# Kernel optimization log

Hardware: AMD Instinct MI355X
Metric: run time of the kernel (lower is better)

Reference implementation:

```python
import jax, jax.numpy as jnp
import numpy as np

STRIDE = 16
NUM_A = 9
POS_TH, NEG_TH = 0.7, 0.3
FG, BG, IGN = 1.0, 0.0, 2.0
CAP = 128  # BATCH_SIZE * 0.5 for both fg and bg


def _generate_base_anchors(base_size=16, ratios=(0.5, 1.0, 2.0), scales=(8, 16, 32)):
    w = h = float(base_size)
    xc = yc = 0.5 * (base_size - 1)
    size = w * h
    out = []
    for r in ratios:
        ws = np.round(np.sqrt(size / r))
        hs = np.round(ws * r)
        for s in scales:
            W, H = ws * s, hs * s
            out.append([xc - 0.5 * (W - 1), yc - 0.5 * (H - 1),
                        xc + 0.5 * (W - 1), yc + 0.5 * (H - 1)])
    return np.asarray(out, dtype=np.float32)  # [9,4]


def _all_anchors(H, W):
    base = _generate_base_anchors()
    sx = np.arange(W, dtype=np.float32) * STRIDE
    sy = np.arange(H, dtype=np.float32) * STRIDE
    xs, ys = np.meshgrid(sx, sy)  # row-major over (h, w)
    shifts = np.stack([xs.ravel(), ys.ravel(), xs.ravel(), ys.ravel()], 1)
    return jnp.asarray((shifts[:, None, :] + base[None, :, :]).reshape(-1, 4))  # [H*W*9,4], order (h,w,a)


def _forward(scores, gt, im_w, im_h):
    H, W = scores.shape[2], scores.shape[3]
    anchors = _all_anchors(H, W)  # [N,4]
    valid = (anchors[:, 0] >= 0.) & (anchors[:, 1] >= 0.) & \
            (anchors[:, 2] < im_w) & (anchors[:, 3] < im_h)
    # pairwise IoU with +1 box convention
    aw = anchors[:, 2] - anchors[:, 0] + 1.
    ah = anchors[:, 3] - anchors[:, 1] + 1.
    a_area = jnp.where((aw > 0) & (ah > 0), aw * ah, 0.)
    gw = gt[:, 2] - gt[:, 0] + 1.
    gh = gt[:, 3] - gt[:, 1] + 1.
    g_area = jnp.where((gw > 0) & (gh > 0), gw * gh, 0.)
    ix1 = jnp.maximum(anchors[:, None, 0], gt[None, :, 0])
    iy1 = jnp.maximum(anchors[:, None, 1], gt[None, :, 1])
    ix2 = jnp.minimum(anchors[:, None, 2], gt[None, :, 2])
    iy2 = jnp.minimum(anchors[:, None, 3], gt[None, :, 3])
    iw = ix2 - ix1 + 1.
    ih = iy2 - iy1 + 1.
    inter = jnp.where((iw > 0) & (ih > 0), iw * ih, 0.)
    ovl = inter / (a_area[:, None] + g_area[None, :] - inter)  # [N,G]
    ovl_m = jnp.where(valid[:, None], ovl, -1.)  # exclude invalid anchors
    a_argmax = jnp.argmax(ovl, axis=1)           # best gt per anchor
    a_max = jnp.max(ovl, axis=1)
    g_max = jnp.max(ovl_m, axis=0)               # best (valid) anchor overlap per gt
    gt_fg = jnp.any(ovl_m == g_max[None, :], axis=1) & valid
    labels = jnp.where(valid & (a_max < NEG_TH), BG, IGN)
    labels = jnp.where(gt_fg, FG, labels)
    labels = jnp.where(valid & (a_max >= POS_TH), FG, labels)
    # random subsample fg/bg down to CAP each (matches npr.choice semantics in distribution)
    kf, kb = jax.random.split(jax.random.key(42))
    def subsample(lbl, mask, k):
        s = jnp.where(mask, jax.random.uniform(k, lbl.shape), jnp.inf)
        ranks = jnp.argsort(jnp.argsort(s))
        keep = ranks < jnp.minimum(jnp.sum(mask), CAP)
        return jnp.where(mask & ~keep, IGN, lbl)
    labels = subsample(labels, labels == FG, kf)
    labels = subsample(labels, labels == BG, kb)
    num_ni = jnp.sum(labels != IGN).astype(jnp.float32)
    gts = gt[a_argmax]
    ax = (anchors[:, 2] + anchors[:, 0]) * 0.5
    ay = (anchors[:, 3] + anchors[:, 1]) * 0.5
    gwm = gts[:, 2] - gts[:, 0] + 1.
    ghm = gts[:, 3] - gts[:, 1] + 1.
    gx = (gts[:, 2] + gts[:, 0]) * 0.5
    gy = (gts[:, 3] + gts[:, 1]) * 0.5
    adj = jnp.stack([(gx - ax) / aw, (gy - ay) / ah,
                     jnp.log(gwm / aw), jnp.log(ghm / ah)], axis=1)  # [N,4]
    adj = jnp.where(valid[:, None], adj, 0.)
    wts = jnp.where((labels == FG)[:, None], 1.0 / num_ni, 0.) * jnp.ones((1, 4), jnp.float32)
    labels_out = labels.reshape(1, H, W, NUM_A).transpose(0, 3, 1, 2) \
                       .reshape(1, 1, NUM_A * H, W).astype(jnp.int32)
    adj_out = adj.reshape(1, H, W, 4 * NUM_A).transpose(0, 3, 1, 2)
    wts_out = wts.reshape(1, H, W, 4 * NUM_A).transpose(0, 3, 1, 2)
    return labels_out, adj_out, wts_out


def setup_inputs() -> dict:
    key = jax.random.key(0)
    k1, k2, k3 = jax.random.split(key, 3)
    scores = jax.random.normal(k1, (1, 18, 256, 256), dtype=jnp.float32)
    G = 64
    cxy = jax.random.uniform(k2, (G, 2), minval=100., maxval=3900.)
    wh = jax.random.uniform(k3, (G, 2), minval=32., maxval=512.)
    x1y1 = jnp.clip(cxy - wh * 0.5, 0., 4095.)
    x2y2 = jnp.clip(cxy + wh * 0.5, 0., 4095.)
    gt = jnp.concatenate([x1y1, x2y2], axis=1)  # [G,4] = x1,y1,x2,y2
    return {"anchor_object_scores": scores, "ground_truth_boxes": gt,
            "im_w": 4096, "im_h": 4096}


def reference(anchor_object_scores, ground_truth_boxes, im_w, im_h):
    return _forward(anchor_object_scores, ground_truth_boxes, im_w, im_h)
```

## Files before the change

kernel.cpp:

```cpp
#include <hip/hip_runtime.h>
#include <stdint.h>


#define NUM_A 9
#define HW 65536
#define N_ANCH 589824
#define NG 64
#define CAPK 128u
#define NBIN 2048
#define BIN_SHIFT 12
#define CAND_CAP 4096
#define NBLK_MAIN 576
#define NBLK_EMIT 576

#define LAB_BG 0u
#define LAB_FG 1u
#define LAB_IGN 2u

#define OFF_GMAX8 0
#define OFF_HF    512
#define OFF_HB    (OFF_HF + NBIN)
#define OFF_CNTF  (OFF_HF + 2*NBIN)
#define OFF_CNTB  (OFF_CNTF + 1)
#define OFF_DONE1 (OFF_CNTF + 2)
#define OFF_SEL   (OFF_CNTF + 8)
#define OFF_CANDF 4624
#define OFF_CANDB (OFF_CANDF + 2*CAND_CAP)
#define OFF_LABM  (OFF_CANDB + 2*CAND_CAP)
#define ZERO_BEG  OFF_HF
#define ZERO_END  OFF_CANDF
#define NZ        (ZERO_END - ZERO_BEG)

__constant__ float BA[NUM_A][4] = {
  { -84.f,  -40.f,  99.f,  55.f}, {-176.f,  -88.f, 191.f, 103.f},
  {-360.f, -184.f, 375.f, 199.f}, { -56.f,  -56.f,  71.f,  71.f},
  {-120.f, -120.f, 135.f, 135.f}, {-248.f, -248.f, 263.f, 263.f},
  { -36.f,  -80.f,  51.f,  95.f}, { -80.f, -168.f,  95.f, 183.f},
  {-168.f, -344.f, 183.f, 359.f}};

__host__ __device__ static inline void tf2x32(uint32_t k0, uint32_t k1,
                                              uint32_t x0, uint32_t x1,
                                              uint32_t* o0, uint32_t* o1) {
  const uint32_t ks2 = k0 ^ k1 ^ 0x1BD11BDAu;
#define TF_R(r) { x0 += x1; x1 = (x1 << (r)) | (x1 >> (32 - (r))); x1 ^= x0; }
  x0 += k0; x1 += k1;
  TF_R(13) TF_R(15) TF_R(26) TF_R(6)
  x0 += k1;  x1 += ks2 + 1u;
  TF_R(17) TF_R(29) TF_R(16) TF_R(24)
  x0 += ks2; x1 += k0 + 2u;
  TF_R(13) TF_R(15) TF_R(26) TF_R(6)
  x0 += k0;  x1 += k1 + 3u;
  TF_R(17) TF_R(29) TF_R(16) TF_R(24)
  x0 += k1;  x1 += ks2 + 4u;
  TF_R(13) TF_R(15) TF_R(26) TF_R(6)
  x0 += ks2; x1 += k0 + 5u;
#undef TF_R
  *o0 = x0; *o1 = x1;
}

__device__ static inline uint32_t mant_of(uint32_t k0, uint32_t k1, uint32_t n) {
  uint32_t o0, o1;
  tf2x32(k0, k1, 0u, n, &o0, &o1);
  return (o0 ^ o1) >> 9;
}

__device__ static inline float iou1(float a0, float a1, float a2, float a3,
                                    float aarea, float g0, float g1, float g2,
                                    float g3, float garea) {
  #pragma clang fp contract(off)
  float ix1 = fmaxf(a0, g0);
  float iy1 = fmaxf(a1, g1);
  float ix2 = fminf(a2, g2);
  float iy2 = fminf(a3, g3);
  float iw = ix2 - ix1 + 1.0f;
  float ih = iy2 - iy1 + 1.0f;
  float inter = (iw > 0.0f && ih > 0.0f) ? iw * ih : 0.0f;
  float den = aarea + garea - inter;
  return inter / den;
}

__global__ __launch_bounds__(256) void k_pre(const float* __restrict__ gt,
                                             const int* __restrict__ imw_p,
                                             const int* __restrict__ imh_p,
                                             uint32_t* __restrict__ ws) {
  #pragma clang fp contract(off)
  int tid = threadIdx.x;
  int b = blockIdx.x;
  int gid = b * 256 + tid;
  if (gid < NZ) ws[ZERO_BEG + gid] = 0u;

  int g = b >> 3, sl = b & 7;
  float g0 = gt[g*4+0], g1 = gt[g*4+1], g2 = gt[g*4+2], g3 = gt[g*4+3];
  float gw = g2 - g0 + 1.0f, gh = g3 - g1 + 1.0f;
  float ga = (gw > 0.0f && gh > 0.0f) ? gw * gh : 0.0f;
  float imw = (float)imw_p[0], imh = (float)imh_p[0];

  float mx = 0.0f;
  for (int a = 0; a < NUM_A; a++) {
    float b0 = BA[a][0], b1 = BA[a][1], b2 = BA[a][2], b3 = BA[a][3];
    int wlo = max(0,   (int)floorf((g0 - 1.0f - b2) * 0.0625f));
    int whi = min(255, (int)ceilf ((g2 + 1.0f - b0) * 0.0625f));
    int hlo = max(0,   (int)floorf((g1 - 1.0f - b3) * 0.0625f));
    int hhi = min(255, (int)ceilf ((g3 + 1.0f - b1) * 0.0625f));
    int wx = whi - wlo + 1, wy = hhi - hlo + 1;
    if (wx <= 0 || wy <= 0) continue;
    int tot = wx * wy;
    for (int idx = sl * 256 + tid; idx < tot; idx += 2048) {
      int h = hlo + idx / wx, w = wlo + idx % wx;
      float sx = (float)(w << 4), sy = (float)(h << 4);
      float x1 = b0 + sx, y1 = b1 + sy, x2 = b2 + sx, y2 = b3 + sy;
      float aw = x2 - x1 + 1.0f, ah = y2 - y1 + 1.0f;
      float aarea = aw * ah;
      bool vld = (x1 >= 0.0f) && (y1 >= 0.0f) && (x2 < imw) && (y2 < imh);
      float o = iou1(x1, y1, x2, y2, aarea, g0, g1, g2, g3, ga);
      if (vld) mx = fmaxf(mx, o);
    }
  }
  #pragma unroll
  for (int s = 32; s >= 1; s >>= 1) mx = fmaxf(mx, __shfl_xor(mx, s, 64));
  __shared__ float wmax[4];
  if ((tid & 63) == 0) wmax[tid >> 6] = mx;
  __syncthreads();
  if (tid == 0) {
    float m = fmaxf(fmaxf(wmax[0], wmax[1]), fmaxf(wmax[2], wmax[3]));
    ws[OFF_GMAX8 + g * 8 + sl] = __float_as_uint(m);
  }
}

__global__ __launch_bounds__(256) void k_main(const float* __restrict__ gt,
                                              const int* __restrict__ imw_p,
                                              const int* __restrict__ imh_p,
                                              float* __restrict__ out_adj,
                                              uint32_t* __restrict__ ws,
                                              uint32_t kf0, uint32_t kf1,
                                              uint32_t kb0, uint32_t kb1) {
  #pragma clang fp contract(off)
  __shared__ float4 sgt4[NG];
  __shared__ float4 cg4[NG];
  __shared__ float2 cgam[NG];
  __shared__ uint32_t crow[NG];
  __shared__ uint32_t sh[2 * NBIN];
  __shared__ int scnt, sAnyZero, sLast;
  int tid = threadIdx.x;
  {
    uint4* sh4 = (uint4*)sh;
    #pragma unroll
    for (int k = 0; k < 4; k++) sh4[tid + k * 256] = make_uint4(0, 0, 0, 0);
  }

  int b = blockIdx.x;
  int a = b >> 6, hb = (b & 63) << 2;
  float BA0 = BA[a][0], BA1 = BA[a][1], BA2 = BA[a][2], BA3 = BA[a][3];

  if (tid < NG) {
    int g = tid;
    const float4 g4 = ((const float4*)gt)[g];
    sgt4[g] = g4;
    float gw = g4.z - g4.x + 1.0f, gh = g4.w - g4.y + 1.0f;
    float ga = (gw > 0.0f && gh > 0.0f) ? gw * gh : 0.0f;
    uint4 q0 = *(const uint4*)&ws[OFF_GMAX8 + g * 8];
    uint4 q1 = *(const uint4*)&ws[OFF_GMAX8 + g * 8 + 4];
    uint32_t mm = max(max(max(q0.x, q0.y), max(q0.z, q0.w)),
                      max(max(q1.x, q1.y), max(q1.z, q1.w)));
    uint32_t rb = 0u;
    #pragma unroll
    for (int r = 0; r < 4; r++) {
      float sy = (float)((hb + r) << 4);
      float ihp = fminf(BA3 + sy, g4.w) - fmaxf(BA1 + sy, g4.y) + 1.0f;
      if (ihp > 0.0f) rb |= (1u << r);
    }
    unsigned long long zb = __ballot(mm == 0u);
    bool pred = (rb != 0u);
    unsigned long long mk = __ballot(pred);
    int idx = __popcll(mk & ((1ull << g) - 1ull));
    if (pred) {
      cg4[idx] = g4;
      cgam[idx] = make_float2(ga, __uint_as_float(mm));
      crow[idx] = (rb << 8) | (uint32_t)g;
    }
    if (g == 0) {
      scnt = __popcll(mk);
      sAnyZero = (zb != 0ull) ? 1 : 0;
    }
  }
  __syncthreads();

  float imw = (float)imw_p[0], imh = (float)imh_p[0];
  int w = tid;
  float sx = (float)(w << 4);
  float A0 = BA0 + sx, A2 = BA2 + sx;
  float aw = A2 - A0 + 1.0f;
  float A1v[4], A3v[4];
  #pragma unroll
  for (int r = 0; r < 4; r++) {
    float sy = (float)((hb + r) << 4);
    A1v[r] = BA1 + sy; A3v[r] = BA3 + sy;
  }
  float ah = A3v[0] - A1v[0] + 1.0f;
  float aarea = aw * ah;
  bool xv = (A0 >= 0.0f) && (A2 < imw);

  int cnt = scnt;
  float amaxv[4] = {0.f, 0.f, 0.f, 0.f};
  int bgv[4] = {0, 0, 0, 0};
  uint32_t afv = 0u;
  for (int i = 0; i < cnt; i++) {
    float4 g4 = cg4[i];
    float iw = fminf(A2, g4.z) - fmaxf(A0, g4.x) + 1.0f;
    if (!__any(iw > 0.0f)) continue;
    float2 gam = cgam[i];
    uint32_t rbg = crow[i];
    if (iw > 0.0f) {
      int g = (int)(rbg & 0xFFu);
      uint32_t rb = rbg >> 8;
      float base = aarea + gam.x;
      float gm = gam.y;
      #pragma unroll
      for (int r = 0; r < 4; r++) {
        if ((rb >> r) & 1u) {
          float ih = fminf(A3v[r], g4.w) - fmaxf(A1v[r], g4.y) + 1.0f;
          float inter = iw * ih;
          float o = inter / (base - inter);
          if (o > amaxv[r]) { amaxv[r] = o; bgv[r] = g; }
          if (o == gm) afv |= (1u << r);
        }
      }
    }
  }

  bool anyZ = (sAnyZero != 0);
  #pragma unroll
  for (int r = 0; r < 4; r++) {
    int hw = (hb + r) * 256 + w;
    bool valid = xv && (A1v[r] >= 0.0f) && (A3v[r] < imh);
    float amax = amaxv[r];
    bool anyfg = (((afv >> r) & 1u) || anyZ) && valid;
    uint32_t lab;
    if (!valid)                       lab = LAB_IGN;
    else if (anyfg || amax >= 0.7f)   lab = LAB_FG;
    else if (amax < 0.3f)             lab = LAB_BG;
    else                              lab = LAB_IGN;

    float adj0 = 0.f, adj1 = 0.f, adj2 = 0.f, adj3 = 0.f;
    if (valid) {
      float4 G = sgt4[bgv[r]];
      float ax = (A2 + A0) * 0.5f, ay = (A3v[r] + A1v[r]) * 0.5f;
      float gwm = G.z - G.x + 1.0f, ghm = G.w - G.y + 1.0f;
      float gx = (G.z + G.x) * 0.5f, gy = (G.w + G.y) * 0.5f;
      adj0 = (gx - ax) / aw;
      adj1 = (gy - ay) / ah;
      adj2 = logf(gwm / aw);
      adj3 = logf(ghm / ah);
    }
    int c4 = a * 4;
    out_adj[(c4 + 0) * HW + hw] = adj0;
    out_adj[(c4 + 1) * HW + hw] = adj1;
    out_adj[(c4 + 2) * HW + hw] = adj2;
    out_adj[(c4 + 3) * HW + hw] = adj3;

    uint32_t m = 0u;
    uint32_t n = (uint32_t)(hw * 9 + a);
    if (lab != LAB_IGN) {
      uint32_t kk0 = (lab == LAB_FG) ? kf0 : kb0;
      uint32_t kk1 = (lab == LAB_FG) ? kf1 : kb1;
      m = mant_of(kk0, kk1, n);
      atomicAdd(&sh[((lab == LAB_FG) ? 0 : NBIN) + (m >> BIN_SHIFT)], 1u);
    }
    ws[OFF_LABM + a * HW + hw] = (lab << 24) | m;
  }

  __syncthreads();
  for (int i = tid; i < 2 * NBIN; i += 256) {
    uint32_t v = sh[i];
    if (v) atomicAdd(&ws[OFF_HF + i], v);
  }
  __syncthreads();
  if (tid == 0) {
    uint32_t prev = __hip_atomic_fetch_add(&ws[OFF_DONE1], 1u,
                                           __ATOMIC_ACQ_REL,
                                           __HIP_MEMORY_SCOPE_AGENT);
    sLast = (prev == NBLK_MAIN - 1u) ? 1 : 0;
  }
  __syncthreads();
  if (sLast) {
    for (int cls = 0; cls < 2; cls++) {
      uint32_t* hist = ws + (cls ? OFF_HB : OFF_HF);
      uint32_t* sel = ws + OFF_SEL + cls * 4;
      uint32_t loc[8], s = 0;
      #pragma unroll
      for (int j = 0; j < 8; j++) {
        loc[j] = __hip_atomic_load(&hist[tid * 8 + j], __ATOMIC_RELAXED,
                                   __HIP_MEMORY_SCOPE_AGENT);
        s += loc[j];
      }
      __syncthreads();
      sh[tid] = s; __syncthreads();
      for (int off = 1; off < 256; off <<= 1) {
        uint32_t v = (tid >= off) ? sh[tid - off] : 0u;
        __syncthreads();
        sh[tid] += v;
        __syncthreads();
      }
      uint32_t total = sh[255];
      uint32_t K = total < CAPK ? total : CAPK;
      if (tid == 0) {
        sel[3] = K;
        if (K == 0u) { sel[0] = 0xFFFFFFFFu; sel[1] = 0u; sel[2] = 0u; }
      }
      if (K > 0u) {
        uint32_t myC = sh[tid], pvC = (tid == 0) ? 0u : sh[tid - 1];
        if (myC >= K && pvC < K) {
          uint32_t cum = pvC; int bb2 = tid * 8;
          for (int j = 0; j < 8; j++) {
            if (cum + loc[j] >= K) { bb2 = tid * 8 + j; break; }
            cum += loc[j];
          }
          sel[0] = (uint32_t)bb2; sel[1] = cum; sel[2] = K - cum;
        }
      }
      __syncthreads();
    }
  }
}

__global__ __launch_bounds__(256) void k_emit(float* __restrict__ out_lab,
                                              float* __restrict__ out_wts,
                                              uint32_t* __restrict__ ws) {
  int tid = threadIdx.x;
  int t4 = (blockIdx.x * 256 + tid) * 4;
  int a = t4 >> 16, hw0 = t4 & 65535;
  uint4 lm4 = *(const uint4*)&ws[OFF_LABM + t4];
  uint32_t bf = ws[OFF_SEL + 0], bbs = ws[OFF_SEL + 4];
  uint32_t Kf = ws[OFF_SEL + 3], Kb = ws[OFF_SEL + 7];
  float inv = 1.0f / (float)(Kf + Kb);
  uint64_t* candf = (uint64_t*)(ws + OFF_CANDF);
  uint64_t* candb = (uint64_t*)(ws + OFF_CANDB);
  uint32_t lane = (uint32_t)(tid & 63);
  unsigned long long below = (1ull << lane) - 1ull;

  float lv[4], wv[4];
  uint32_t lms[4] = {lm4.x, lm4.y, lm4.z, lm4.w};
  #pragma unroll
  for (int j = 0; j < 4; j++) {
    uint32_t lab = lms[j] >> 24;
    uint32_t m = lms[j] & 0x7FFFFFu;
    uint32_t bn = m >> BIN_SHIFT;
    float outv = 2.0f, wvv = 0.0f;
    bool pushf = false, pushb = false;
    if (lab == LAB_FG) {
      if (bn < bf) { outv = 1.0f; wvv = inv; }
      else if (bn == bf) pushf = true;
    } else if (lab == LAB_BG) {
      if (bn < bbs) { outv = 0.0f; }
      else if (bn == bbs) pushb = true;
    }
    unsigned long long mkf = __ballot(pushf);
    if (mkf) {
      uint32_t c = (uint32_t)__popcll(mkf);
      int leader = __ffsll(mkf) - 1;
      uint32_t base = 0;
      if ((int)lane == leader) base = atomicAdd(&ws[OFF_CNTF], c);
      base = (uint32_t)__shfl((int)base, leader, 64);
      if (pushf) {
        uint32_t idx = base + (uint32_t)__popcll(mkf & below);
        if (idx < CAND_CAP) {
          uint32_t n = (uint32_t)((hw0 + j) * 9 + a);
          candf[idx] = ((uint64_t)m << 20) | (uint64_t)n;
        }
      }
    }
    unsigned long long mkb = __ballot(pushb);
    if (mkb) {
      uint32_t c = (uint32_t)__popcll(mkb);
      int leader = __ffsll(mkb) - 1;
      uint32_t base = 0;
      if ((int)lane == leader) base = atomicAdd(&ws[OFF_CNTB], c);
      base = (uint32_t)__shfl((int)base, leader, 64);
      if (pushb) {
        uint32_t idx = base + (uint32_t)__popcll(mkb & below);
        if (idx < CAND_CAP) {
          uint32_t n = (uint32_t)((hw0 + j) * 9 + a);
          candb[idx] = ((uint64_t)m << 20) | (uint64_t)n;
        }
      }
    }
    lv[j] = outv; wv[j] = wvv;
  }
  *(float4*)&out_lab[t4] = make_float4(lv[0], lv[1], lv[2], lv[3]);
  float4 wq = make_float4(wv[0], wv[1], wv[2], wv[3]);
  int c4 = a * 4;
  *(float4*)&out_wts[(c4 + 0) * HW + hw0] = wq;
  *(float4*)&out_wts[(c4 + 1) * HW + hw0] = wq;
  *(float4*)&out_wts[(c4 + 2) * HW + hw0] = wq;
  *(float4*)&out_wts[(c4 + 3) * HW + hw0] = wq;
}

__global__ __launch_bounds__(256) void k_fixup(float* __restrict__ out_lab,
                                               float* __restrict__ out_wts,
                                               uint32_t* __restrict__ ws) {
  __shared__ uint64_t sc[CAND_CAP];
  int cls = blockIdx.x;
  uint32_t cnt = ws[cls == 0 ? OFF_CNTF : OFF_CNTB];
  uint32_t C = cnt < CAND_CAP ? cnt : CAND_CAP;
  uint32_t need = ws[OFF_SEL + cls * 4 + 2];
  uint32_t Kf = ws[OFF_SEL + 3], Kb = ws[OFF_SEL + 7];
  float inv = 1.0f / (float)(Kf + Kb);
  const uint64_t* cand =
      (const uint64_t*)(ws + (cls == 0 ? OFF_CANDF : OFF_CANDB));
  for (uint32_t i = threadIdx.x; i < C; i += 256) sc[i] = cand[i];
  __syncthreads();
  for (uint32_t i = threadIdx.x; i < C; i += 256) {
    uint64_t k = sc[i];
    uint32_t r = 0;
    for (uint32_t j = 0; j < C; j++) r += (sc[j] < k) ? 1u : 0u;
    if (r < need) {
      uint32_t n = (uint32_t)(k & 0xFFFFFu);
      uint32_t aa = n % 9u, hw = n / 9u;
      uint32_t t = aa * HW + hw;
      if (cls == 0) {
        out_lab[t] = 1.0f;
        #pragma unroll
        for (int j = 0; j < 4; j++) out_wts[(aa * 4 + j) * HW + hw] = inv;
      } else {
        out_lab[t] = 0.0f;
      }
    }
  }
}

extern "C" void kernel_launch(void* const* d_in, const int* in_sizes, int n_in,
                              void* d_out, int out_size, void* d_ws,
                              size_t ws_size, hipStream_t stream) {
  const float* gt  = (const float*)d_in[1];
  const int*   imw = (const int*)d_in[2];
  const int*   imh = (const int*)d_in[3];
  float* out      = (float*)d_out;
  float* out_lab  = out;
  float* out_adj  = out + N_ANCH;
  float* out_wts  = out + 5 * N_ANCH;
  uint32_t* ws = (uint32_t*)d_ws;

  uint32_t kf0, kf1, kb0, kb1;
  tf2x32(0u, 42u, 0u, 0u, &kf0, &kf1);
  tf2x32(0u, 42u, 0u, 1u, &kb0, &kb1);

  hipLaunchKernelGGL(k_pre, dim3(NG * 8), dim3(256), 0, stream, gt, imw, imh,
                     ws);
  hipLaunchKernelGGL(k_main, dim3(NBLK_MAIN), dim3(256), 0, stream, gt, imw,
                     imh, out_adj, ws, kf0, kf1, kb0, kb1);
  hipLaunchKernelGGL(k_emit, dim3(NBLK_EMIT), dim3(256), 0, stream, out_lab,
                     out_wts, ws);
  hipLaunchKernelGGL(k_fixup, dim3(2), dim3(256), 0, stream, out_lab, out_wts,
                     ws);
}
```

Before: 110.3 us.

## Fuse emit and fixup into main kernel via candidate lists and last-block selection

```diff
diff --git a/kernel.cpp b/kernel.cpp
--- a/kernel.cpp
+++ b/kernel.cpp
@@ -7,29 +7,22 @@
 #define N_ANCH 589824
 #define NG 64
 #define CAPK 128u
-#define NBIN 2048
-#define BIN_SHIFT 12
 #define CAND_CAP 4096
 #define NBLK_MAIN 576
-#define NBLK_EMIT 576
+#define T_BG 32768u
 
 #define LAB_BG 0u
 #define LAB_FG 1u
 #define LAB_IGN 2u
 
 #define OFF_GMAX8 0
-#define OFF_HF    512
-#define OFF_HB    (OFF_HF + NBIN)
-#define OFF_CNTF  (OFF_HF + 2*NBIN)
-#define OFF_CNTB  (OFF_CNTF + 1)
-#define OFF_DONE1 (OFF_CNTF + 2)
-#define OFF_SEL   (OFF_CNTF + 8)
-#define OFF_CANDF 4624
+#define OFF_CNTF  512
+#define OFF_CNTB  513
+#define OFF_TOTBG 514
+#define OFF_DONE  515
+#define OFF_CANDF 520
 #define OFF_CANDB (OFF_CANDF + 2*CAND_CAP)
 #define OFF_LABM  (OFF_CANDB + 2*CAND_CAP)
-#define ZERO_BEG  OFF_HF
-#define ZERO_END  OFF_CANDF
-#define NZ        (ZERO_END - ZERO_BEG)
 
 __constant__ float BA[NUM_A][4] = {
   { -84.f,  -40.f,  99.f,  55.f}, {-176.f,  -88.f, 191.f, 103.f},
@@ -64,6 +57,33 @@
   return (o0 ^ o1) >> 9;
 }
 
+__device__ static inline uint32_t agload(const uint32_t* p) {
+  return __hip_atomic_load(p, __ATOMIC_RELAXED, __HIP_MEMORY_SCOPE_AGENT);
+}
+__device__ static inline uint64_t agload64(const uint64_t* p) {
+  return __hip_atomic_load(p, __ATOMIC_RELAXED, __HIP_MEMORY_SCOPE_AGENT);
+}
+__device__ static inline void agstore(uint32_t* p, uint32_t v) {
+  __hip_atomic_store(p, v, __ATOMIC_RELAXED, __HIP_MEMORY_SCOPE_AGENT);
+}
+__device__ static inline void agstore64(uint64_t* p, uint64_t v) {
+  __hip_atomic_store(p, v, __ATOMIC_RELAXED, __HIP_MEMORY_SCOPE_AGENT);
+}
+
+__device__ static inline void write_kept(int cls, uint32_t n, float inv,
+                                         float* __restrict__ out_lab,
+                                         float* __restrict__ out_wts) {
+  uint32_t aa = n % 9u, hw = n / 9u;
+  uint32_t t = aa * HW + hw;
+  if (cls == 0) {
+    out_lab[t] = 1.0f;
+    #pragma unroll
+    for (int j = 0; j < 4; j++) out_wts[(aa * 4 + j) * HW + hw] = inv;
+  } else {
+    out_lab[t] = 0.0f;
+  }
+}
+
 __device__ static inline float iou1(float a0, float a1, float a2, float a3,
                                     float aarea, float g0, float g1, float g2,
                                     float g3, float garea) {
@@ -86,8 +106,7 @@
   #pragma clang fp contract(off)
   int tid = threadIdx.x;
   int b = blockIdx.x;
-  int gid = b * 256 + tid;
-  if (gid < NZ) ws[ZERO_BEG + gid] = 0u;
+  if (b == 0 && tid < 8) ws[512 + tid] = 0u;
 
   int g = b >> 3, sl = b & 7;
   float g0 = gt[g*4+0], g1 = gt[g*4+1], g2 = gt[g*4+2], g3 = gt[g*4+3];
@@ -130,7 +149,9 @@
 __global__ __launch_bounds__(256) void k_main(const float* __restrict__ gt,
                                               const int* __restrict__ imw_p,
                                               const int* __restrict__ imh_p,
+                                              float* __restrict__ out_lab,
                                               float* __restrict__ out_adj,
+                                              float* __restrict__ out_wts,
                                               uint32_t* __restrict__ ws,
                                               uint32_t kf0, uint32_t kf1,
                                               uint32_t kb0, uint32_t kb1) {
@@ -139,19 +160,18 @@
   __shared__ float4 cg4[NG];
   __shared__ float2 cgam[NG];
   __shared__ uint32_t crow[NG];
-  __shared__ uint32_t sh[2 * NBIN];
   __shared__ int scnt, sAnyZero, sLast;
+  __shared__ uint32_t sTotBG, sbf, sneed, sBcnt;
+  __shared__ uint32_t sscan[256];
+  __shared__ uint32_t shist[2048];
+  __shared__ uint64_t scand[CAND_CAP];
   int tid = threadIdx.x;
-  {
-    uint4* sh4 = (uint4*)sh;
-    #pragma unroll
-    for (int k = 0; k < 4; k++) sh4[tid + k * 256] = make_uint4(0, 0, 0, 0);
-  }
 
   int b = blockIdx.x;
   int a = b >> 6, hb = (b & 63) << 2;
   float BA0 = BA[a][0], BA1 = BA[a][1], BA2 = BA[a][2], BA3 = BA[a][3];
 
+  if (tid == 0) { sTotBG = 0u; }
   if (tid < NG) {
     int g = tid;
     const float4 g4 = ((const float4*)gt)[g];
@@ -229,6 +249,12 @@
   }
 
   bool anyZ = (sAnyZero != 0);
+  uint64_t* candf = (uint64_t*)(ws + OFF_CANDF);
+  uint64_t* candb = (uint64_t*)(ws + OFF_CANDB);
+  uint32_t lane = (uint32_t)(tid & 63);
+  unsigned long long below = (1ull << lane) - 1ull;
+  uint32_t bgc = 0u;
+
   #pragma unroll
   for (int r = 0; r < 4; r++) {
     int hw = (hb + r) * 256 + w;
@@ -257,6 +283,11 @@
     out_adj[(c4 + 1) * HW + hw] = adj1;
     out_adj[(c4 + 2) * HW + hw] = adj2;
     out_adj[(c4 + 3) * HW + hw] = adj3;
+    out_lab[a * HW + hw] = 2.0f;
+    out_wts[(c4 + 0) * HW + hw] = 0.0f;
+    out_wts[(c4 + 1) * HW + hw] = 0.0f;
+    out_wts[(c4 + 2) * HW + hw] = 0.0f;
+    out_wts[(c4 + 3) * HW + hw] = 0.0f;
 
     uint32_t m = 0u;
     uint32_t n = (uint32_t)(hw * 9 + a);
@@ -264,96 +295,13 @@
       uint32_t kk0 = (lab == LAB_FG) ? kf0 : kb0;
       uint32_t kk1 = (lab == LAB_FG) ? kf1 : kb1;
       m = mant_of(kk0, kk1, n);
-      atomicAdd(&sh[((lab == LAB_FG) ? 0 : NBIN) + (m >> BIN_SHIFT)], 1u);
-    }
-    ws[OFF_LABM + a * HW + hw] = (lab << 24) | m;
-  }
-
-  __syncthreads();
-  for (int i = tid; i < 2 * NBIN; i += 256) {
-    uint32_t v = sh[i];
-    if (v) atomicAdd(&ws[OFF_HF + i], v);
-  }
-  __syncthreads();
-  if (tid == 0) {
-    uint32_t prev = __hip_atomic_fetch_add(&ws[OFF_DONE1], 1u,
-                                           __ATOMIC_ACQ_REL,
-                                           __HIP_MEMORY_SCOPE_AGENT);
-    sLast = (prev == NBLK_MAIN - 1u) ? 1 : 0;
-  }
-  __syncthreads();
-  if (sLast) {
-    for (int cls = 0; cls < 2; cls++) {
-      uint32_t* hist = ws + (cls ? OFF_HB : OFF_HF);
-      uint32_t* sel = ws + OFF_SEL + cls * 4;
-      uint32_t loc[8], s = 0;
-      #pragma unroll
-      for (int j = 0; j < 8; j++) {
-        loc[j] = __hip_atomic_load(&hist[tid * 8 + j], __ATOMIC_RELAXED,
-                                   __HIP_MEMORY_SCOPE_AGENT);
-        s += loc[j];
-      }
-      __syncthreads();
-      sh[tid] = s; __syncthreads();
-      for (int off = 1; off < 256; off <<= 1) {
-        uint32_t v = (tid >= off) ? sh[tid - off] : 0u;
-        __syncthreads();
-        sh[tid] += v;
-        __syncthreads();
-      }
-      uint32_t total = sh[255];
-      uint32_t K = total < CAPK ? total : CAPK;
-      if (tid == 0) {
-        sel[3] = K;
-        if (K == 0u) { sel[0] = 0xFFFFFFFFu; sel[1] = 0u; sel[2] = 0u; }
-      }
-      if (K > 0u) {
-        uint32_t myC = sh[tid], pvC = (tid == 0) ? 0u : sh[tid - 1];
-        if (myC >= K && pvC < K) {
-          uint32_t cum = pvC; int bb2 = tid * 8;
-          for (int j = 0; j < 8; j++) {
-            if (cum + loc[j] >= K) { bb2 = tid * 8 + j; break; }
-            cum += loc[j];
-          }
-          sel[0] = (uint32_t)bb2; sel[1] = cum; sel[2] = K - cum;
-        }
-      }
-      __syncthreads();
-    }
-  }
-}
-
-__global__ __launch_bounds__(256) void k_emit(float* __restrict__ out_lab,
-                                              float* __restrict__ out_wts,
-                                              uint32_t* __restrict__ ws) {
-  int tid = threadIdx.x;
-  int t4 = (blockIdx.x * 256 + tid) * 4;
-  int a = t4 >> 16, hw0 = t4 & 65535;
-  uint4 lm4 = *(const uint4*)&ws[OFF_LABM + t4];
-  uint32_t bf = ws[OFF_SEL + 0], bbs = ws[OFF_SEL + 4];
-  uint32_t Kf = ws[OFF_SEL + 3], Kb = ws[OFF_SEL + 7];
-  float inv = 1.0f / (float)(Kf + Kb);
-  uint64_t* candf = (uint64_t*)(ws + OFF_CANDF);
-  uint64_t* candb = (uint64_t*)(ws + OFF_CANDB);
-  uint32_t lane = (uint32_t)(tid & 63);
-  unsigned long long below = (1ull << lane) - 1ull;
-
-  float lv[4], wv[4];
-  uint32_t lms[4] = {lm4.x, lm4.y, lm4.z, lm4.w};
-  #pragma unroll
-  for (int j = 0; j < 4; j++) {
-    uint32_t lab = lms[j] >> 24;
-    uint32_t m = lms[j] & 0x7FFFFFu;
-    uint32_t bn = m >> BIN_SHIFT;
-    float outv = 2.0f, wvv = 0.0f;
-    bool pushf = false, pushb = false;
-    if (lab == LAB_FG) {
-      if (bn < bf) { outv = 1.0f; wvv = inv; }
-      else if (bn == bf) pushf = true;
-    } else if (lab == LAB_BG) {
-      if (bn < bbs) { outv = 0.0f; }
-      else if (bn == bbs) pushb = true;
-    }
+    }
+    agstore(&ws[OFF_LABM + a * HW + hw], (lab << 24) | m);
+    bgc += (lab == LAB_BG) ? 1u : 0u;
+
+    bool pushf = (lab == LAB_FG);
+    bool pushb = (lab == LAB_BG) && (m < T_BG);
+    uint64_t key = ((uint64_t)m << 20) | (uint64_t)n;
     unsigned long long mkf = __ballot(pushf);
     if (mkf) {
       uint32_t c = (uint32_t)__popcll(mkf);
@@ -363,10 +311,7 @@
       base = (uint32_t)__shfl((int)base, leader, 64);
       if (pushf) {
         uint32_t idx = base + (uint32_t)__popcll(mkf & below);
-        if (idx < CAND_CAP) {
-          uint32_t n = (uint32_t)((hw0 + j) * 9 + a);
-          candf[idx] = ((uint64_t)m << 20) | (uint64_t)n;
-        }
+        if (idx < CAND_CAP) agstore64(&candf[idx], key);
       }
     }
     unsigned long long mkb = __ballot(pushb);
@@ -378,52 +323,127 @@
       base = (uint32_t)__shfl((int)base, leader, 64);
       if (pushb) {
         uint32_t idx = base + (uint32_t)__popcll(mkb & below);
-        if (idx < CAND_CAP) {
-          uint32_t n = (uint32_t)((hw0 + j) * 9 + a);
-          candb[idx] = ((uint64_t)m << 20) | (uint64_t)n;
+        if (idx < CAND_CAP) agstore64(&candb[idx], key);
+      }
+    }
+  }
+
+  #pragma unroll
+  for (int s2 = 32; s2 >= 1; s2 >>= 1)
+    bgc += (uint32_t)__shfl_xor((int)bgc, s2, 64);
+  if ((tid & 63) == 0) atomicAdd(&sTotBG, bgc);
+  __syncthreads();
+  if (tid == 0) {
+    atomicAdd(&ws[OFF_TOTBG], sTotBG);
+    uint32_t prev = __hip_atomic_fetch_add(&ws[OFF_DONE], 1u,
+                                           __ATOMIC_ACQ_REL,
+                                           __HIP_MEMORY_SCOPE_AGENT);
+    sLast = (prev == NBLK_MAIN - 1u) ? 1 : 0;
+  }
+  __syncthreads();
+
+  if (sLast) {
+    uint32_t cntF = agload(&ws[OFF_CNTF]);
+    uint32_t cntB = agload(&ws[OFF_CNTB]);
+    uint32_t totB = agload(&ws[OFF_TOTBG]);
+    uint32_t Kf = cntF < CAPK ? cntF : CAPK;
+    uint32_t Kb = totB < CAPK ? totB : CAPK;
+    float inv = 1.0f / (float)(Kf + Kb);
+    for (int cls = 0; cls < 2; cls++) {
+      uint32_t K = cls ? Kb : Kf;
+      uint32_t C = cls ? cntB : cntF;
+      uint32_t clsLab = cls ? LAB_BG : LAB_FG;
+      bool fast = (C <= CAND_CAP) && (C >= K);
+      for (uint32_t i = tid; i < 2048; i += 256) shist[i] = 0u;
+      if (tid == 0) { sbf = 0u; sneed = 0u; sBcnt = 0u; }
+      __syncthreads();
+      if (fast) {
+        const uint64_t* gc = cls ? candb : candf;
+        for (uint32_t i = tid; i < C; i += 256) {
+          uint64_t k = agload64(&gc[i]);
+          scand[i] = k;
+          atomicAdd(&shist[(uint32_t)(k >> 32)], 1u);
         }
-      }
-    }
-    lv[j] = outv; wv[j] = wvv;
-  }
-  *(float4*)&out_lab[t4] = make_float4(lv[0], lv[1], lv[2], lv[3]);
-  float4 wq = make_float4(wv[0], wv[1], wv[2], wv[3]);
-  int c4 = a * 4;
-  *(float4*)&out_wts[(c4 + 0) * HW + hw0] = wq;
-  *(float4*)&out_wts[(c4 + 1) * HW + hw0] = wq;
-  *(float4*)&out_wts[(c4 + 2) * HW + hw0] = wq;
-  *(float4*)&out_wts[(c4 + 3) * HW + hw0] = wq;
-}
-
-__global__ __launch_bounds__(256) void k_fixup(float* __restrict__ out_lab,
-                                               float* __restrict__ out_wts,
-                                               uint32_t* __restrict__ ws) {
-  __shared__ uint64_t sc[CAND_CAP];
-  int cls = blockIdx.x;
-  uint32_t cnt = ws[cls == 0 ? OFF_CNTF : OFF_CNTB];
-  uint32_t C = cnt < CAND_CAP ? cnt : CAND_CAP;
-  uint32_t need = ws[OFF_SEL + cls * 4 + 2];
-  uint32_t Kf = ws[OFF_SEL + 3], Kb = ws[OFF_SEL + 7];
-  float inv = 1.0f / (float)(Kf + Kb);
-  const uint64_t* cand =
-      (const uint64_t*)(ws + (cls == 0 ? OFF_CANDF : OFF_CANDB));
-  for (uint32_t i = threadIdx.x; i < C; i += 256) sc[i] = cand[i];
-  __syncthreads();
-  for (uint32_t i = threadIdx.x; i < C; i += 256) {
-    uint64_t k = sc[i];
-    uint32_t r = 0;
-    for (uint32_t j = 0; j < C; j++) r += (sc[j] < k) ? 1u : 0u;
-    if (r < need) {
-      uint32_t n = (uint32_t)(k & 0xFFFFFu);
-      uint32_t aa = n % 9u, hw = n / 9u;
-      uint32_t t = aa * HW + hw;
-      if (cls == 0) {
-        out_lab[t] = 1.0f;
-        #pragma unroll
-        for (int j = 0; j < 4; j++) out_wts[(aa * 4 + j) * HW + hw] = inv;
       } else {
-        out_lab[t] = 0.0f;
-      }
+        for (uint32_t t2 = tid; t2 < N_ANCH; t2 += 256) {
+          uint32_t lm = agload(&ws[OFF_LABM + t2]);
+          if ((lm >> 24) == clsLab)
+            atomicAdd(&shist[(lm & 0x7FFFFFu) >> 12], 1u);
+        }
+      }
+      __syncthreads();
+      uint32_t loc[8], s = 0;
+      #pragma unroll
+      for (int j = 0; j < 8; j++) { loc[j] = shist[tid * 8 + j]; s += loc[j]; }
+      sscan[tid] = s;
+      __syncthreads();
+      for (int off = 1; off < 256; off <<= 1) {
+        uint32_t v = (tid >= off) ? sscan[tid - off] : 0u;
+        __syncthreads();
+        sscan[tid] += v;
+        __syncthreads();
+      }
+      if (K > 0u) {
+        uint32_t myC = sscan[tid], pvC = (tid == 0) ? 0u : sscan[tid - 1];
+        if (myC >= K && pvC < K) {
+          uint32_t cum = pvC; uint32_t bb2 = tid * 8;
+          for (int j = 0; j < 8; j++) {
+            if (cum + loc[j] >= K) { bb2 = tid * 8 + j; break; }
+            cum += loc[j];
+          }
+          sbf = bb2 + 1u;
+          sneed = K - cum;
+        }
+      }
+      __syncthreads();
+      uint32_t bfp1 = sbf, need = sneed;
+      if (bfp1 > 0u) {
+        uint32_t bf = bfp1 - 1u;
+        if (fast) {
+          for (uint32_t i = tid; i < C; i += 256) {
+            uint64_t k = scand[i];
+            uint32_t bin = (uint32_t)(k >> 32);
+            bool keep = false;
+            if (bin < bf) keep = true;
+            else if (bin == bf) {
+              uint32_t r = 0;
+              for (uint32_t j = 0; j < C; j++) {
+                uint64_t o = scand[j];
+                r += ((uint32_t)(o >> 32) == bf && o < k) ? 1u : 0u;
+              }
+              keep = (r < need);
+            }
+            if (keep)
+              write_kept(cls, (uint32_t)(k & 0xFFFFFu), inv, out_lab, out_wts);
+          }
+        } else {
+          for (uint32_t t2 = tid; t2 < N_ANCH; t2 += 256) {
+            uint32_t lm = agload(&ws[OFF_LABM + t2]);
+            if ((lm >> 24) != clsLab) continue;
+            uint32_t m = lm & 0x7FFFFFu;
+            uint32_t bin = m >> 12;
+            if (bin > bf) continue;
+            uint32_t n = (uint32_t)((t2 & 65535) * 9 + (t2 >> 16));
+            if (bin < bf) {
+              write_kept(cls, n, inv, out_lab, out_wts);
+            } else {
+              uint32_t idx = atomicAdd(&sBcnt, 1u);
+              if (idx < CAND_CAP)
+                scand[idx] = ((uint64_t)m << 20) | (uint64_t)n;
+            }
+          }
+          __syncthreads();
+          uint32_t Cb = sBcnt < CAND_CAP ? sBcnt : CAND_CAP;
+          for (uint32_t i = tid; i < Cb; i += 256) {
+            uint64_t k = scand[i];
+            uint32_t r = 0;
+            for (uint32_t j = 0; j < Cb; j++) r += (scand[j] < k) ? 1u : 0u;
+            if (r < need)
+              write_kept(cls, (uint32_t)(k & 0xFFFFFu), inv, out_lab, out_wts);
+          }
+        }
+      }
+      __syncthreads();
     }
   }
 }
@@ -447,9 +467,5 @@
   hipLaunchKernelGGL(k_pre, dim3(NG * 8), dim3(256), 0, stream, gt, imw, imh,
                      ws);
   hipLaunchKernelGGL(k_main, dim3(NBLK_MAIN), dim3(256), 0, stream, gt, imw,
-                     imh, out_adj, ws, kf0, kf1, kb0, kb1);
-  hipLaunchKernelGGL(k_emit, dim3(NBLK_EMIT), dim3(256), 0, stream, out_lab,
-                     out_wts, ws);
-  hipLaunchKernelGGL(k_fixup, dim3(2), dim3(256), 0, stream, out_lab, out_wts,
-                     ws);
-}
+                     imh, out_lab, out_adj, out_wts, ws, kf0, kf1, kb0, kb1);
+}
```

After: 432.9 us. 293% more time.
